# Kernel tuning notes

Hardware: AMD Instinct MI355X
Metric: run time of the kernel (lower is better)

## Reference

```python
import jax, jax.numpy as jnp
import numpy as np

B, D_IN, H = 4096, 2048, 2048


def setup_inputs() -> dict:
    key = jax.random.key(0)
    ks = jax.random.split(key, 8)
    s = 0.07
    return {
        "inputs": jax.random.normal(ks[0], (B, D_IN), dtype=jnp.float32),
        "state": jax.random.normal(ks[1], (B, H), dtype=jnp.float32),
        "theta_u_w": jax.random.uniform(ks[2], (H, H), jnp.float32, -s, s),
        "theta_w_w": jax.random.uniform(ks[3], (D_IN, H), jnp.float32, -s, s),
        "theta_w_b": jnp.ones((H,), jnp.float32),
        "eta_u_w": jax.random.uniform(ks[4], (H, H), jnp.float32, -s, s),
        "eta_w_w": jax.random.uniform(ks[5], (D_IN, H), jnp.float32, -s, s),
        "eta_w_b": -jnp.ones((H,), jnp.float32),
        "wx_w": jax.random.uniform(ks[6], (D_IN, H), jnp.float32, -s, s),
    }


def reference(inputs, state, theta_u_w, theta_w_w, theta_w_b,
              eta_u_w, eta_w_w, eta_w_b, wx_w):
    # Forget gate: sigmoid(state @ Wtu + inputs @ Wtw + btw)
    theta = jax.nn.sigmoid(state @ theta_u_w + inputs @ theta_w_w + theta_w_b)
    # Input gate: sigmoid(state @ Weu + inputs @ Wew + bew)
    eta = jax.nn.sigmoid(state @ eta_u_w + inputs @ eta_w_w + eta_w_b)
    Wx = inputs @ wx_w
    h = theta * jnp.tanh(state) + eta * jnp.tanh(Wx)
    return (h, h)
```

## Files before the change

kernel.cpp:

```cpp
#include <hip/hip_runtime.h>
#include <hip/hip_bf16.h>

#define BATCH 4096
#define KD    2048
#define HD    2048

typedef float f32x4 __attribute__((ext_vector_type(4)));
typedef short bf16x8 __attribute__((ext_vector_type(8)));

__device__ __forceinline__ unsigned short f2bf(float f) {
  unsigned int u = __builtin_bit_cast(unsigned int, f);
  u = (u + 0x7fffu + ((u >> 16) & 1u)) >> 16;
  return (unsigned short)u;
}

__device__ __forceinline__ float fsigmoid(float x) { return 1.0f / (1.0f + __expf(-x)); }
__device__ __forceinline__ float ftanh(float x) {
  return 1.0f - 2.0f / (__expf(2.0f * x) + 1.0f);
}

__device__ __forceinline__ void gload16(const void* g, void* l) {
  __builtin_amdgcn_global_load_lds(
      (const __attribute__((address_space(1))) unsigned int*)(uintptr_t)g,
      (__attribute__((address_space(3))) unsigned int*)(uintptr_t)l, 16, 0, 0);
}

#define WS_NEED   75497472ull
#define OFF_STATE (16ull << 20)
#define OFF_W     (32ull << 20)

__global__ __launch_bounds__(256) void act_convert(
    const float* __restrict__ inputs, const float* __restrict__ state,
    char* __restrict__ dst) {
  unsigned gid = blockIdx.x * 256 + threadIdx.x;
  const float* src = inputs;
  char* d = dst;
  unsigned id = gid;
  if (gid >= (1u << 20)) { src = state; d = dst + OFF_STATE; id = gid - (1u << 20); }
  const unsigned cid = id & 1023, panel = id >> 10;
  const unsigned kb = panel & 31, rb = panel >> 5;
  const unsigned x = cid * 16, r = x >> 7, xb = x & 127;
  const unsigned k0 = (xb ^ ((r & 7) << 4)) >> 1;
  const float* s = src + (size_t)(rb * 128 + r) * KD + kb * 64 + k0;
  const float4 v0 = *reinterpret_cast<const float4*>(s);
  const float4 v1 = *reinterpret_cast<const float4*>(s + 4);
  uint4 w;
  w.x = (unsigned)f2bf(v0.x) | ((unsigned)f2bf(v0.y) << 16);
  w.y = (unsigned)f2bf(v0.z) | ((unsigned)f2bf(v0.w) << 16);
  w.z = (unsigned)f2bf(v1.x) | ((unsigned)f2bf(v1.y) << 16);
  w.w = (unsigned)f2bf(v1.z) | ((unsigned)f2bf(v1.w) << 16);
  *reinterpret_cast<uint4*>(d + (size_t)id * 16) = w;
}

__global__ __launch_bounds__(256) void weight_convert(
    const float* __restrict__ tu, const float* __restrict__ eu,
    const float* __restrict__ tw, const float* __restrict__ ew,
    const float* __restrict__ xw, char* __restrict__ dst) {
  __shared__ float tile[64][129];
  const int tid = threadIdx.x;
  const int b = blockIdx.x;
  const int w = b >> 9, panel = b & 511;
  const int nb = panel >> 5, kb = panel & 31;
  const float* W = (w == 0) ? tu : (w == 1) ? eu : (w == 2) ? tw : (w == 3) ? ew : xw;
#pragma unroll
  for (int i = 0; i < 8; ++i) {
    const int idx = i * 256 + tid;
    const int row = idx >> 5, c4 = idx & 31;
    const float4 v = *reinterpret_cast<const float4*>(
        W + (size_t)(kb * 64 + row) * HD + nb * 128 + c4 * 4);
    tile[row][c4 * 4 + 0] = v.x; tile[row][c4 * 4 + 1] = v.y;
    tile[row][c4 * 4 + 2] = v.z; tile[row][c4 * 4 + 3] = v.w;
  }
  __syncthreads();
  char* d = dst + OFF_W + ((size_t)(w * 512 + panel) << 14);
#pragma unroll
  for (int i = 0; i < 4; ++i) {
    const int cid = i * 256 + tid;
    const int n = cid >> 3, xb = (cid & 7) * 16;
    const int k0 = (xb ^ ((n & 7) << 4)) >> 1;
    uint4 ww;
    ww.x = (unsigned)f2bf(tile[k0 + 0][n]) | ((unsigned)f2bf(tile[k0 + 1][n]) << 16);
    ww.y = (unsigned)f2bf(tile[k0 + 2][n]) | ((unsigned)f2bf(tile[k0 + 3][n]) << 16);
    ww.z = (unsigned)f2bf(tile[k0 + 4][n]) | ((unsigned)f2bf(tile[k0 + 5][n]) << 16);
    ww.w = (unsigned)f2bf(tile[k0 + 6][n]) | ((unsigned)f2bf(tile[k0 + 7][n]) << 16);
    *reinterpret_cast<uint4*>(d + n * 128 + xb) = ww;
  }
}

__global__ __launch_bounds__(256, 2) void cfn_main(
    const char* __restrict__ ws, const float* __restrict__ state,
    const float* __restrict__ th_b, const float* __restrict__ et_b,
    float* __restrict__ out) {
  __shared__ char sm[65536];
  const int tid = threadIdx.x;
  int bid = blockIdx.x;
  bid = (bid & 7) * 64 + (bid >> 3);
  const int bx = bid & 15, by = bid >> 4;
  const int lane = tid & 63, wv = tid >> 6;
  const int wr = wv >> 1, wc = wv & 1;
  const int lr = lane & 15, lg = lane >> 4;
  const int t16 = tid * 16;

  const char* pAx = ws;
  const char* pAs = ws + OFF_STATE;
  const char* pW  = ws + OFF_W;

  f32x4 at[4][4], ae[4][4], ax[4][4];
#pragma unroll
  for (int m = 0; m < 4; ++m)
#pragma unroll
    for (int n = 0; n < 4; ++n)
#pragma unroll
      for (int v = 0; v < 4; ++v) { at[m][n][v] = 0.f; ae[m][n][v] = 0.f; ax[m][n][v] = 0.f; }

  for (int kb = 0; kb < 32; ++kb) {
    const char* ga = pAs + ((size_t)(by * 32 + kb) << 14);
    const char* g0 = pW + ((size_t)(0 * 512 + bx * 32 + kb) << 14);
    const char* g1 = pW + ((size_t)(1 * 512 + bx * 32 + kb) << 14);
#pragma unroll
    for (int i = 0; i < 4; ++i) {
      gload16(ga + t16 + i * 4096, sm + t16 + i * 4096);
      gload16(g0 + t16 + i * 4096, sm + 16384 + t16 + i * 4096);
      gload16(g1 + t16 + i * 4096, sm + 32768 + t16 + i * 4096);
    }
    __syncthreads();
#pragma unroll
    for (int kk = 0; kk < 2; ++kk) {
      const int kc = kk * 64 + lg * 16;
      bf16x8 a[4], b[4];
#pragma unroll
      for (int m = 0; m < 4; ++m) {
        const int r = wr * 64 + m * 16 + lr;
        a[m] = *reinterpret_cast<const bf16x8*>(sm + r * 128 + (kc ^ ((r & 7) << 4)));
      }
#pragma unroll
      for (int n = 0; n < 4; ++n) {
        const int c = wc * 64 + n * 16 + lr;
        b[n] = *reinterpret_cast<const bf16x8*>(sm + 16384 + c * 128 + (kc ^ ((c & 7) << 4)));
      }
#pragma unroll
      for (int m = 0; m < 4; ++m)
#pragma unroll
        for (int n = 0; n < 4; ++n)
          at[m][n] = __builtin_amdgcn_mfma_f32_16x16x32_bf16(a[m], b[n], at[m][n], 0, 0, 0);
#pragma unroll
      for (int n = 0; n < 4; ++n) {
        const int c = wc * 64 + n * 16 + lr;
        b[n] = *reinterpret_cast<const bf16x8*>(sm + 32768 + c * 128 + (kc ^ ((c & 7) << 4)));
      }
#pragma unroll
      for (int m = 0; m < 4; ++m)
#pragma unroll
        for (int n = 0; n < 4; ++n)
          ae[m][n] = __builtin_amdgcn_mfma_f32_16x16x32_bf16(a[m], b[n], ae[m][n], 0, 0, 0);
    }
    __syncthreads();
  }

  for (int kb = 0; kb < 32; ++kb) {
    const char* ga = pAx + ((size_t)(by * 32 + kb) << 14);
    const char* g0 = pW + ((size_t)(2 * 512 + bx * 32 + kb) << 14);
    const char* g1 = pW + ((size_t)(3 * 512 + bx * 32 + kb) << 14);
    const char* g2 = pW + ((size_t)(4 * 512 + bx * 32 + kb) << 14);
#pragma unroll
    for (int i = 0; i < 4; ++i) {
      gload16(ga + t16 + i * 4096, sm + t16 + i * 4096);
      gload16(g0 + t16 + i * 4096, sm + 16384 + t16 + i * 4096);
      gload16(g1 + t16 + i * 4096, sm + 32768 + t16 + i * 4096);
      gload16(g2 + t16 + i * 4096, sm + 49152 + t16 + i * 4096);
    }
    __syncthreads();
#pragma unroll
    for (int kk = 0; kk < 2; ++kk) {
      const int kc = kk * 64 + lg * 16;
      bf16x8 a[4], b[4];
#pragma unroll
      for (int m = 0; m < 4; ++m) {
        const int r = wr * 64 + m * 16 + lr;
        a[m] = *reinterpret_cast<const bf16x8*>(sm + r * 128 + (kc ^ ((r & 7) << 4)));
      }
#pragma unroll
      for (int n = 0; n < 4; ++n) {
        const int c = wc * 64 + n * 16 + lr;
        b[n] = *reinterpret_cast<const bf16x8*>(sm + 16384 + c * 128 + (kc ^ ((c & 7) << 4)));
      }
#pragma unroll
      for (int m = 0; m < 4; ++m)
#pragma unroll
        for (int n = 0; n < 4; ++n)
          at[m][n] = __builtin_amdgcn_mfma_f32_16x16x32_bf16(a[m], b[n], at[m][n], 0, 0, 0);
#pragma unroll
      for (int n = 0; n < 4; ++n) {
        const int c = wc * 64 + n * 16 + lr;
        b[n] = *reinterpret_cast<const bf16x8*>(sm + 32768 + c * 128 + (kc ^ ((c & 7) << 4)));
      }
#pragma unroll
      for (int m = 0; m < 4; ++m)
#pragma unroll
        for (int n = 0; n < 4; ++n)
          ae[m][n] = __builtin_amdgcn_mfma_f32_16x16x32_bf16(a[m], b[n], ae[m][n], 0, 0, 0);
#pragma unroll
      for (int n = 0; n < 4; ++n) {
        const int c = wc * 64 + n * 16 + lr;
        b[n] = *reinterpret_cast<const bf16x8*>(sm + 49152 + c * 128 + (kc ^ ((c & 7) << 4)));
      }
#pragma unroll
      for (int m = 0; m < 4; ++m)
#pragma unroll
        for (int n = 0; n < 4; ++n)
          ax[m][n] = __builtin_amdgcn_mfma_f32_16x16x32_bf16(a[m], b[n], ax[m][n], 0, 0, 0);
    }
    __syncthreads();
  }

  float* const out2 = out + (size_t)BATCH * HD;
  const int n0 = bx * 128, m0 = by * 128;
#pragma unroll
  for (int n = 0; n < 4; ++n) {
    const int c = n0 + wc * 64 + n * 16 + lr;
    const float tb = th_b[c], eb = et_b[c];
#pragma unroll
    for (int m = 0; m < 4; ++m) {
#pragma unroll
      for (int v = 0; v < 4; ++v) {
        const int r = m0 + wr * 64 + m * 16 + lg * 4 + v;
        const float st = state[(size_t)r * HD + c];
        const float h = fsigmoid(at[m][n][v] + tb) * ftanh(st)
                      + fsigmoid(ae[m][n][v] + eb) * ftanh(ax[m][n][v]);
        out[(size_t)r * HD + c] = h;
        out2[(size_t)r * HD + c] = h;
      }
    }
  }
}

__global__ __launch_bounds__(256, 2) void cfn_fallback(
    const float* __restrict__ inputs, const float* __restrict__ state,
    const float* __restrict__ th_u, const float* __restrict__ th_w,
    const float* __restrict__ th_b, const float* __restrict__ et_u,
    const float* __restrict__ et_w, const float* __restrict__ et_b,
    const float* __restrict__ wx_w, float* __restrict__ out) {
  __shared__ unsigned short sA[128 * 64];
  __shared__ unsigned short sB[128 * 64];
  char* const sAb = (char*)sA;
  char* const sBb = (char*)sB;
  const int tid = threadIdx.x;
  const int n0 = blockIdx.x * 128;
  const int m0 = blockIdx.y * 128;
  const int lane = tid & 63, wv = tid >> 6;
  const int wr = wv >> 1, wc = wv & 1;
  const int lr = lane & 15, lg = lane >> 4;
  const int a_kq = tid & 15, a_mb = tid >> 4;
  const int b_n = tid & 127, b_k8 = (tid >> 7) * 8;
  f32x4 acc[4][4], r2[4][4];
  auto zero_acc = [&]() {
#pragma unroll
    for (int m = 0; m < 4; ++m)
#pragma unroll
      for (int n = 0; n < 4; ++n) {
        acc[m][n][0] = 0.f; acc[m][n][1] = 0.f; acc[m][n][2] = 0.f; acc[m][n][3] = 0.f;
      }
  };
  auto gemm_seg = [&](const float* __restrict__ Ap, const float* __restrict__ Wp) {
    for (int k0 = 0; k0 < KD; k0 += 64) {
#pragma unroll
      for (int p = 0; p < 8; ++p) {
        const int m = p * 16 + a_mb;
        const float4 v = *reinterpret_cast<const float4*>(
            Ap + (size_t)(m0 + m) * KD + k0 + a_kq * 4);
        uint2 w;
        w.x = (unsigned)f2bf(v.x) | ((unsigned)f2bf(v.y) << 16);
        w.y = (unsigned)f2bf(v.z) | ((unsigned)f2bf(v.w) << 16);
        const int byte = m * 128 + ((a_kq * 8) ^ ((m & 7) << 4));
        *reinterpret_cast<uint2*>(sAb + byte) = w;
      }
#pragma unroll
      for (int p = 0; p < 4; ++p) {
        const int kb = p * 16 + b_k8;
        const float* bp = Wp + (size_t)(k0 + kb) * HD + n0 + b_n;
        uint4 w;
        w.x = (unsigned)f2bf(bp[0 * HD]) | ((unsigned)f2bf(bp[1 * HD]) << 16);
        w.y = (unsigned)f2bf(bp[2 * HD]) | ((unsigned)f2bf(bp[3 * HD]) << 16);
        w.z = (unsigned)f2bf(bp[4 * HD]) | ((unsigned)f2bf(bp[5 * HD]) << 16);
        w.w = (unsigned)f2bf(bp[6 * HD]) | ((unsigned)f2bf(bp[7 * HD]) << 16);
        const int byte = b_n * 128 + ((kb * 2) ^ ((b_n & 7) << 4));
        *reinterpret_cast<uint4*>(sBb + byte) = w;
      }
      __syncthreads();
#pragma unroll
      for (int kk = 0; kk < 2; ++kk) {
        bf16x8 af[4], bfr[4];
#pragma unroll
        for (int m = 0; m < 4; ++m) {
          const int r = wr * 64 + m * 16 + lr;
          af[m] = *reinterpret_cast<const bf16x8*>(sAb + r * 128 + ((kk * 64 + lg * 16) ^ ((r & 7) << 4)));
        }
#pragma unroll
        for (int n = 0; n < 4; ++n) {
          const int c = wc * 64 + n * 16 + lr;
          bfr[n] = *reinterpret_cast<const bf16x8*>(sBb + c * 128 + ((kk * 64 + lg * 16) ^ ((c & 7) << 4)));
        }
#pragma unroll
        for (int m = 0; m < 4; ++m)
#pragma unroll
          for (int n = 0; n < 4; ++n)
            acc[m][n] = __builtin_amdgcn_mfma_f32_16x16x32_bf16(af[m], bfr[n], acc[m][n], 0, 0, 0);
      }
      __syncthreads();
    }
  };
  zero_acc();
  gemm_seg(state, et_u);
  gemm_seg(inputs, et_w);
#pragma unroll
  for (int n = 0; n < 4; ++n) {
    const int c = n0 + wc * 64 + n * 16 + lr;
    const float eb = et_b[c];
#pragma unroll
    for (int m = 0; m < 4; ++m)
#pragma unroll
      for (int v = 0; v < 4; ++v) r2[m][n][v] = fsigmoid(acc[m][n][v] + eb);
  }
  zero_acc();
  gemm_seg(inputs, wx_w);
#pragma unroll
  for (int m = 0; m < 4; ++m)
#pragma unroll
    for (int n = 0; n < 4; ++n)
#pragma unroll
      for (int v = 0; v < 4; ++v) r2[m][n][v] *= ftanh(acc[m][n][v]);
  zero_acc();
  gemm_seg(state, th_u);
  gemm_seg(inputs, th_w);
  float* const out2 = out + (size_t)BATCH * HD;
#pragma unroll
  for (int n = 0; n < 4; ++n) {
    const int c = n0 + wc * 64 + n * 16 + lr;
    const float tb = th_b[c];
#pragma unroll
    for (int m = 0; m < 4; ++m)
#pragma unroll
      for (int v = 0; v < 4; ++v) {
        const int r = m0 + wr * 64 + m * 16 + lg * 4 + v;
        const float st = state[(size_t)r * HD + c];
        const float h = fsigmoid(acc[m][n][v] + tb) * ftanh(st) + r2[m][n][v];
        out[(size_t)r * HD + c] = h;
        out2[(size_t)r * HD + c] = h;
      }
  }
}

extern "C" void kernel_launch(void* const* d_in, const int* in_sizes, int n_in,
                              void* d_out, int out_size, void* d_ws, size_t ws_size,
                              hipStream_t stream) {
  const float* inputs = (const float*)d_in[0];
  const float* state  = (const float*)d_in[1];
  const float* th_u   = (const float*)d_in[2];
  const float* th_w   = (const float*)d_in[3];
  const float* th_b   = (const float*)d_in[4];
  const float* et_u   = (const float*)d_in[5];
  const float* et_w   = (const float*)d_in[6];
  const float* et_b   = (const float*)d_in[7];
  const float* wx_w   = (const float*)d_in[8];
  float* out = (float*)d_out;

  if (ws_size < WS_NEED) {
    dim3 grid(HD / 128, BATCH / 128);
    hipLaunchKernelGGL(cfn_fallback, grid, dim3(256), 0, stream,
                       inputs, state, th_u, th_w, th_b, et_u, et_w, et_b, wx_w, out);
    return;
  }

  char* ws = (char*)d_ws;
  hipLaunchKernelGGL(act_convert, dim3(8192), dim3(256), 0, stream, inputs, state, ws);
  hipLaunchKernelGGL(weight_convert, dim3(2560), dim3(256), 0, stream,
                     th_u, et_u, th_w, et_w, wx_w, ws);
  hipLaunchKernelGGL(cfn_main, dim3(512), dim3(256), 0, stream,
                     ws, state, th_b, et_b, out);
}
```

Measured before the change: 189.8 us.

## Enlarge main GEMM tile to 256x128 with 512 threads and double-buffered LDS

```diff
diff --git a/kernel.cpp b/kernel.cpp
--- a/kernel.cpp
+++ b/kernel.cpp
@@ -87,17 +87,17 @@
   }
 }
 
-__global__ __launch_bounds__(256, 2) void cfn_main(
+__global__ __launch_bounds__(512, 2) void cfn_main(
     const char* __restrict__ ws, const float* __restrict__ state,
     const float* __restrict__ th_b, const float* __restrict__ et_b,
     float* __restrict__ out) {
-  __shared__ char sm[65536];
+  __shared__ char sm[163840];
   const int tid = threadIdx.x;
   int bid = blockIdx.x;
-  bid = (bid & 7) * 64 + (bid >> 3);
+  bid = (bid & 7) * 32 + (bid >> 3);
   const int bx = bid & 15, by = bid >> 4;
   const int lane = tid & 63, wv = tid >> 6;
-  const int wr = wv >> 1, wc = wv & 1;
+  const int wm = wv >> 2, wn = wv & 3;
   const int lr = lane & 15, lg = lane >> 4;
   const int t16 = tid * 16;
 
@@ -105,125 +105,119 @@
   const char* pAs = ws + OFF_STATE;
   const char* pW  = ws + OFF_W;
 
-  f32x4 at[4][4], ae[4][4], ax[4][4];
-#pragma unroll
-  for (int m = 0; m < 4; ++m)
-#pragma unroll
-    for (int n = 0; n < 4; ++n)
+  f32x4 at[8][2], ae[8][2], ax[8][2];
+#pragma unroll
+  for (int m = 0; m < 8; ++m)
+#pragma unroll
+    for (int n = 0; n < 2; ++n)
 #pragma unroll
       for (int v = 0; v < 4; ++v) { at[m][n][v] = 0.f; ae[m][n][v] = 0.f; ax[m][n][v] = 0.f; }
 
-  for (int kb = 0; kb < 32; ++kb) {
-    const char* ga = pAs + ((size_t)(by * 32 + kb) << 14);
-    const char* g0 = pW + ((size_t)(0 * 512 + bx * 32 + kb) << 14);
-    const char* g1 = pW + ((size_t)(1 * 512 + bx * 32 + kb) << 14);
-#pragma unroll
-    for (int i = 0; i < 4; ++i) {
-      gload16(ga + t16 + i * 4096, sm + t16 + i * 4096);
-      gload16(g0 + t16 + i * 4096, sm + 16384 + t16 + i * 4096);
-      gload16(g1 + t16 + i * 4096, sm + 32768 + t16 + i * 4096);
-    }
+  auto stage = [&](int t, char* dst) {
+    const int kb = t & 31;
+    const char* Asrc = (t < 32) ? pAs : pAx;
+    const int w0 = (t < 32) ? 0 : 2;
+    const int nB = (t < 32) ? 2 : 3;
+    const char* pa = Asrc + (((size_t)(by * 64 + kb)) << 14);
+#pragma unroll
+    for (int s = 0; s < 2; ++s)
+#pragma unroll
+      for (int j = 0; j < 2; ++j)
+        gload16(pa + s * (32 << 14) + t16 + j * 8192,
+                dst + s * 16384 + t16 + j * 8192);
+#pragma unroll
+    for (int p = 0; p < 3; ++p) {
+      if (p < nB) {
+        const char* pb = pW + (((size_t)((w0 + p) * 512 + bx * 32 + kb)) << 14);
+#pragma unroll
+        for (int j = 0; j < 2; ++j)
+          gload16(pb + t16 + j * 8192, dst + 32768 + p * 16384 + t16 + j * 8192);
+      }
+    }
+  };
+
+  auto compute2 = [&](const char* buf) {
+#pragma unroll
+    for (int kk = 0; kk < 2; ++kk) {
+      const int swz = (kk * 64 + lg * 16) ^ ((lr & 7) << 4);
+      bf16x8 b0[2], b1[2];
+#pragma unroll
+      for (int n = 0; n < 2; ++n) {
+        const int c = wn * 32 + n * 16 + lr;
+        b0[n] = *reinterpret_cast<const bf16x8*>(buf + 32768 + c * 128 + swz);
+        b1[n] = *reinterpret_cast<const bf16x8*>(buf + 49152 + c * 128 + swz);
+      }
+#pragma unroll
+      for (int m = 0; m < 8; ++m) {
+        const int r = wm * 128 + m * 16 + lr;
+        const bf16x8 a = *reinterpret_cast<const bf16x8*>(buf + r * 128 + swz);
+#pragma unroll
+        for (int n = 0; n < 2; ++n) {
+          at[m][n] = __builtin_amdgcn_mfma_f32_16x16x32_bf16(a, b0[n], at[m][n], 0, 0, 0);
+          ae[m][n] = __builtin_amdgcn_mfma_f32_16x16x32_bf16(a, b1[n], ae[m][n], 0, 0, 0);
+        }
+      }
+    }
+  };
+
+  auto compute3 = [&](const char* buf) {
+#pragma unroll
+    for (int kk = 0; kk < 2; ++kk) {
+      const int swz = (kk * 64 + lg * 16) ^ ((lr & 7) << 4);
+      bf16x8 b0[2], b1[2], b2[2];
+#pragma unroll
+      for (int n = 0; n < 2; ++n) {
+        const int c = wn * 32 + n * 16 + lr;
+        b0[n] = *reinterpret_cast<const bf16x8*>(buf + 32768 + c * 128 + swz);
+        b1[n] = *reinterpret_cast<const bf16x8*>(buf + 49152 + c * 128 + swz);
+        b2[n] = *reinterpret_cast<const bf16x8*>(buf + 65536 + c * 128 + swz);
+      }
+#pragma unroll
+      for (int m = 0; m < 8; ++m) {
+        const int r = wm * 128 + m * 16 + lr;
+        const bf16x8 a = *reinterpret_cast<const bf16x8*>(buf + r * 128 + swz);
+#pragma unroll
+        for (int n = 0; n < 2; ++n) {
+          at[m][n] = __builtin_amdgcn_mfma_f32_16x16x32_bf16(a, b0[n], at[m][n], 0, 0, 0);
+          ae[m][n] = __builtin_amdgcn_mfma_f32_16x16x32_bf16(a, b1[n], ae[m][n], 0, 0, 0);
+          ax[m][n] = __builtin_amdgcn_mfma_f32_16x16x32_bf16(a, b2[n], ax[m][n], 0, 0, 0);
+        }
+      }
+    }
+  };
+
+  char* cur = sm;
+  char* nxt = sm + 81920;
+  stage(0, cur);
+  __syncthreads();
+
+  for (int t = 0; t < 32; ++t) {
+    stage(t + 1, nxt);
+    compute2(cur);
+    asm volatile("s_waitcnt vmcnt(0)" ::: "memory");
     __syncthreads();
-#pragma unroll
-    for (int kk = 0; kk < 2; ++kk) {
-      const int kc = kk * 64 + lg * 16;
-      bf16x8 a[4], b[4];
-#pragma unroll
-      for (int m = 0; m < 4; ++m) {
-        const int r = wr * 64 + m * 16 + lr;
-        a[m] = *reinterpret_cast<const bf16x8*>(sm + r * 128 + (kc ^ ((r & 7) << 4)));
-      }
-#pragma unroll
-      for (int n = 0; n < 4; ++n) {
-        const int c = wc * 64 + n * 16 + lr;
-        b[n] = *reinterpret_cast<const bf16x8*>(sm + 16384 + c * 128 + (kc ^ ((c & 7) << 4)));
-      }
-#pragma unroll
-      for (int m = 0; m < 4; ++m)
-#pragma unroll
-        for (int n = 0; n < 4; ++n)
-          at[m][n] = __builtin_amdgcn_mfma_f32_16x16x32_bf16(a[m], b[n], at[m][n], 0, 0, 0);
-#pragma unroll
-      for (int n = 0; n < 4; ++n) {
-        const int c = wc * 64 + n * 16 + lr;
-        b[n] = *reinterpret_cast<const bf16x8*>(sm + 32768 + c * 128 + (kc ^ ((c & 7) << 4)));
-      }
-#pragma unroll
-      for (int m = 0; m < 4; ++m)
-#pragma unroll
-        for (int n = 0; n < 4; ++n)
-          ae[m][n] = __builtin_amdgcn_mfma_f32_16x16x32_bf16(a[m], b[n], ae[m][n], 0, 0, 0);
-    }
+    char* tmp = cur; cur = nxt; nxt = tmp;
+  }
+  for (int t = 32; t < 64; ++t) {
+    if (t < 63) stage(t + 1, nxt);
+    compute3(cur);
+    asm volatile("s_waitcnt vmcnt(0)" ::: "memory");
     __syncthreads();
-  }
-
-  for (int kb = 0; kb < 32; ++kb) {
-    const char* ga = pAx + ((size_t)(by * 32 + kb) << 14);
-    const char* g0 = pW + ((size_t)(2 * 512 + bx * 32 + kb) << 14);
-    const char* g1 = pW + ((size_t)(3 * 512 + bx * 32 + kb) << 14);
-    const char* g2 = pW + ((size_t)(4 * 512 + bx * 32 + kb) << 14);
-#pragma unroll
-    for (int i = 0; i < 4; ++i) {
-      gload16(ga + t16 + i * 4096, sm + t16 + i * 4096);
-      gload16(g0 + t16 + i * 4096, sm + 16384 + t16 + i * 4096);
-      gload16(g1 + t16 + i * 4096, sm + 32768 + t16 + i * 4096);
-      gload16(g2 + t16 + i * 4096, sm + 49152 + t16 + i * 4096);
-    }
-    __syncthreads();
-#pragma unroll
-    for (int kk = 0; kk < 2; ++kk) {
-      const int kc = kk * 64 + lg * 16;
-      bf16x8 a[4], b[4];
-#pragma unroll
-      for (int m = 0; m < 4; ++m) {
-        const int r = wr * 64 + m * 16 + lr;
-        a[m] = *reinterpret_cast<const bf16x8*>(sm + r * 128 + (kc ^ ((r & 7) << 4)));
-      }
-#pragma unroll
-      for (int n = 0; n < 4; ++n) {
-        const int c = wc * 64 + n * 16 + lr;
-        b[n] = *reinterpret_cast<const bf16x8*>(sm + 16384 + c * 128 + (kc ^ ((c & 7) << 4)));
-      }
-#pragma unroll
-      for (int m = 0; m < 4; ++m)
-#pragma unroll
-        for (int n = 0; n < 4; ++n)
-          at[m][n] = __builtin_amdgcn_mfma_f32_16x16x32_bf16(a[m], b[n], at[m][n], 0, 0, 0);
-#pragma unroll
-      for (int n = 0; n < 4; ++n) {
-        const int c = wc * 64 + n * 16 + lr;
-        b[n] = *reinterpret_cast<const bf16x8*>(sm + 32768 + c * 128 + (kc ^ ((c & 7) << 4)));
-      }
-#pragma unroll
-      for (int m = 0; m < 4; ++m)
-#pragma unroll
-        for (int n = 0; n < 4; ++n)
-          ae[m][n] = __builtin_amdgcn_mfma_f32_16x16x32_bf16(a[m], b[n], ae[m][n], 0, 0, 0);
-#pragma unroll
-      for (int n = 0; n < 4; ++n) {
-        const int c = wc * 64 + n * 16 + lr;
-        b[n] = *reinterpret_cast<const bf16x8*>(sm + 49152 + c * 128 + (kc ^ ((c & 7) << 4)));
-      }
-#pragma unroll
-      for (int m = 0; m < 4; ++m)
-#pragma unroll
-        for (int n = 0; n < 4; ++n)
-          ax[m][n] = __builtin_amdgcn_mfma_f32_16x16x32_bf16(a[m], b[n], ax[m][n], 0, 0, 0);
-    }
-    __syncthreads();
+    char* tmp = cur; cur = nxt; nxt = tmp;
   }
 
   float* const out2 = out + (size_t)BATCH * HD;
-  const int n0 = bx * 128, m0 = by * 128;
-#pragma unroll
-  for (int n = 0; n < 4; ++n) {
-    const int c = n0 + wc * 64 + n * 16 + lr;
+  const int n0 = bx * 128 + wn * 32;
+  const int m0 = by * 256 + wm * 128;
+#pragma unroll
+  for (int n = 0; n < 2; ++n) {
+    const int c = n0 + n * 16 + lr;
     const float tb = th_b[c], eb = et_b[c];
 #pragma unroll
-    for (int m = 0; m < 4; ++m) {
+    for (int m = 0; m < 8; ++m) {
 #pragma unroll
       for (int v = 0; v < 4; ++v) {
-        const int r = m0 + wr * 64 + m * 16 + lg * 4 + v;
+        const int r = m0 + m * 16 + lg * 4 + v;
         const float st = state[(size_t)r * HD + c];
         const float h = fsigmoid(at[m][n][v] + tb) * ftanh(st)
                       + fsigmoid(ae[m][n][v] + eb) * ftanh(ax[m][n][v]);
@@ -375,6 +369,6 @@
   hipLaunchKernelGGL(act_convert, dim3(8192), dim3(256), 0, stream, inputs, state, ws);
   hipLaunchKernelGGL(weight_convert, dim3(2560), dim3(256), 0, stream,
                      th_u, et_u, th_w, et_w, wx_w, ws);
-  hipLaunchKernelGGL(cfn_main, dim3(512), dim3(256), 0, stream,
+  hipLaunchKernelGGL(cfn_main, dim3(256), dim3(512), 0, stream,
                      ws, state, th_b, et_b, out);
 }
```

Measured after the change: 202.3 us. 1.07x slower.

## Double-buffer LDS with 32-wide K panels to overlap loads and MFMA

Applied to the files above, without the earlier changes.

```diff
diff --git a/kernel.cpp b/kernel.cpp
--- a/kernel.cpp
+++ b/kernel.cpp
@@ -37,11 +37,11 @@
   char* d = dst;
   unsigned id = gid;
   if (gid >= (1u << 20)) { src = state; d = dst + OFF_STATE; id = gid - (1u << 20); }
-  const unsigned cid = id & 1023, panel = id >> 10;
-  const unsigned kb = panel & 31, rb = panel >> 5;
-  const unsigned x = cid * 16, r = x >> 7, xb = x & 127;
-  const unsigned k0 = (xb ^ ((r & 7) << 4)) >> 1;
-  const float* s = src + (size_t)(rb * 128 + r) * KD + kb * 64 + k0;
+  const unsigned cid = id & 511, panel = id >> 9;
+  const unsigned kb = panel & 63, rb = panel >> 6;
+  const unsigned x = cid * 16, r = x >> 6, xb = x & 63;
+  const unsigned k0 = (xb ^ ((r & 3) << 4)) >> 1;
+  const float* s = src + (size_t)(rb * 128 + r) * KD + kb * 32 + k0;
   const float4 v0 = *reinterpret_cast<const float4*>(s);
   const float4 v1 = *reinterpret_cast<const float4*>(s + 4);
   uint4 w;
@@ -59,31 +59,33 @@
   __shared__ float tile[64][129];
   const int tid = threadIdx.x;
   const int b = blockIdx.x;
-  const int w = b >> 9, panel = b & 511;
-  const int nb = panel >> 5, kb = panel & 31;
+  const int w = b >> 9, blk = b & 511;
+  const int nb = blk >> 5, kb2 = blk & 31;
   const float* W = (w == 0) ? tu : (w == 1) ? eu : (w == 2) ? tw : (w == 3) ? ew : xw;
 #pragma unroll
   for (int i = 0; i < 8; ++i) {
     const int idx = i * 256 + tid;
     const int row = idx >> 5, c4 = idx & 31;
     const float4 v = *reinterpret_cast<const float4*>(
-        W + (size_t)(kb * 64 + row) * HD + nb * 128 + c4 * 4);
+        W + (size_t)(kb2 * 64 + row) * HD + nb * 128 + c4 * 4);
     tile[row][c4 * 4 + 0] = v.x; tile[row][c4 * 4 + 1] = v.y;
     tile[row][c4 * 4 + 2] = v.z; tile[row][c4 * 4 + 3] = v.w;
   }
   __syncthreads();
-  char* d = dst + OFF_W + ((size_t)(w * 512 + panel) << 14);
 #pragma unroll
   for (int i = 0; i < 4; ++i) {
-    const int cid = i * 256 + tid;
-    const int n = cid >> 3, xb = (cid & 7) * 16;
-    const int k0 = (xb ^ ((n & 7) << 4)) >> 1;
+    const int cg = i * 256 + tid;
+    const int half = cg >> 9, cid = cg & 511;
+    const int n = cid >> 2, xb = (cid & 3) * 16;
+    const int k0 = (xb ^ ((n & 3) << 4)) >> 1;
+    char* d = dst + OFF_W +
+        ((size_t)(w * 1024 + nb * 64 + kb2 * 2 + half) << 13);
     uint4 ww;
-    ww.x = (unsigned)f2bf(tile[k0 + 0][n]) | ((unsigned)f2bf(tile[k0 + 1][n]) << 16);
-    ww.y = (unsigned)f2bf(tile[k0 + 2][n]) | ((unsigned)f2bf(tile[k0 + 3][n]) << 16);
-    ww.z = (unsigned)f2bf(tile[k0 + 4][n]) | ((unsigned)f2bf(tile[k0 + 5][n]) << 16);
-    ww.w = (unsigned)f2bf(tile[k0 + 6][n]) | ((unsigned)f2bf(tile[k0 + 7][n]) << 16);
-    *reinterpret_cast<uint4*>(d + n * 128 + xb) = ww;
+    ww.x = (unsigned)f2bf(tile[half * 32 + k0 + 0][n]) | ((unsigned)f2bf(tile[half * 32 + k0 + 1][n]) << 16);
+    ww.y = (unsigned)f2bf(tile[half * 32 + k0 + 2][n]) | ((unsigned)f2bf(tile[half * 32 + k0 + 3][n]) << 16);
+    ww.z = (unsigned)f2bf(tile[half * 32 + k0 + 4][n]) | ((unsigned)f2bf(tile[half * 32 + k0 + 5][n]) << 16);
+    ww.w = (unsigned)f2bf(tile[half * 32 + k0 + 6][n]) | ((unsigned)f2bf(tile[half * 32 + k0 + 7][n]) << 16);
+    *reinterpret_cast<uint4*>(d + n * 64 + xb) = ww;
   }
 }
 
@@ -100,6 +102,7 @@
   const int wr = wv >> 1, wc = wv & 1;
   const int lr = lane & 15, lg = lane >> 4;
   const int t16 = tid * 16;
+  const int swz = (lg * 16) ^ ((lr & 3) << 4);
 
   const char* pAx = ws;
   const char* pAs = ws + OFF_STATE;
@@ -113,105 +116,88 @@
 #pragma unroll
       for (int v = 0; v < 4; ++v) { at[m][n][v] = 0.f; ae[m][n][v] = 0.f; ax[m][n][v] = 0.f; }
 
-  for (int kb = 0; kb < 32; ++kb) {
-    const char* ga = pAs + ((size_t)(by * 32 + kb) << 14);
-    const char* g0 = pW + ((size_t)(0 * 512 + bx * 32 + kb) << 14);
-    const char* g1 = pW + ((size_t)(1 * 512 + bx * 32 + kb) << 14);
-#pragma unroll
-    for (int i = 0; i < 4; ++i) {
-      gload16(ga + t16 + i * 4096, sm + t16 + i * 4096);
-      gload16(g0 + t16 + i * 4096, sm + 16384 + t16 + i * 4096);
-      gload16(g1 + t16 + i * 4096, sm + 32768 + t16 + i * 4096);
-    }
+  auto stage = [&](int t, char* dst) {
+    const int kb = t & 63;
+    const char* Asrc = (t < 64) ? pAs : pAx;
+    const int w0 = (t < 64) ? 0 : 2;
+    const int nB = (t < 64) ? 2 : 3;
+    const char* pa = Asrc + ((size_t)(by * 64 + kb) << 13);
+    gload16(pa + t16, dst + t16);
+    gload16(pa + t16 + 4096, dst + t16 + 4096);
+#pragma unroll
+    for (int p = 0; p < 3; ++p) {
+      if (p < nB) {
+        const char* pb = pW + ((size_t)((w0 + p) * 1024 + bx * 64 + kb) << 13);
+        gload16(pb + t16, dst + 8192 + p * 8192 + t16);
+        gload16(pb + t16 + 4096, dst + 8192 + p * 8192 + t16 + 4096);
+      }
+    }
+  };
+
+  auto compute2 = [&](const char* buf) {
+    bf16x8 a[4], b0[4], b1[4];
+#pragma unroll
+    for (int m = 0; m < 4; ++m) {
+      const int r = wr * 64 + m * 16 + lr;
+      a[m] = *reinterpret_cast<const bf16x8*>(buf + r * 64 + swz);
+    }
+#pragma unroll
+    for (int n = 0; n < 4; ++n) {
+      const int c = wc * 64 + n * 16 + lr;
+      b0[n] = *reinterpret_cast<const bf16x8*>(buf + 8192 + c * 64 + swz);
+      b1[n] = *reinterpret_cast<const bf16x8*>(buf + 16384 + c * 64 + swz);
+    }
+#pragma unroll
+    for (int m = 0; m < 4; ++m)
+#pragma unroll
+      for (int n = 0; n < 4; ++n) {
+        at[m][n] = __builtin_amdgcn_mfma_f32_16x16x32_bf16(a[m], b0[n], at[m][n], 0, 0, 0);
+        ae[m][n] = __builtin_amdgcn_mfma_f32_16x16x32_bf16(a[m], b1[n], ae[m][n], 0, 0, 0);
+      }
+  };
+
+  auto compute3 = [&](const char* buf) {
+    bf16x8 a[4], b0[4], b1[4], b2[4];
+#pragma unroll
+    for (int m = 0; m < 4; ++m) {
+      const int r = wr * 64 + m * 16 + lr;
+      a[m] = *reinterpret_cast<const bf16x8*>(buf + r * 64 + swz);
+    }
+#pragma unroll
+    for (int n = 0; n < 4; ++n) {
+      const int c = wc * 64 + n * 16 + lr;
+      b0[n] = *reinterpret_cast<const bf16x8*>(buf + 8192 + c * 64 + swz);
+      b1[n] = *reinterpret_cast<const bf16x8*>(buf + 16384 + c * 64 + swz);
+      b2[n] = *reinterpret_cast<const bf16x8*>(buf + 24576 + c * 64 + swz);
+    }
+#pragma unroll
+    for (int m = 0; m < 4; ++m)
+#pragma unroll
+      for (int n = 0; n < 4; ++n) {
+        at[m][n] = __builtin_amdgcn_mfma_f32_16x16x32_bf16(a[m], b0[n], at[m][n], 0, 0, 0);
+        ae[m][n] = __builtin_amdgcn_mfma_f32_16x16x32_bf16(a[m], b1[n], ae[m][n], 0, 0, 0);
+        ax[m][n] = __builtin_amdgcn_mfma_f32_16x16x32_bf16(a[m], b2[n], ax[m][n], 0, 0, 0);
+      }
+  };
+
+  char* cur = sm;
+  char* nxt = sm + 32768;
+  stage(0, cur);
+  __syncthreads();
+
+  for (int t = 0; t < 64; ++t) {
+    stage(t + 1, nxt);
+    compute2(cur);
     __syncthreads();
-#pragma unroll
-    for (int kk = 0; kk < 2; ++kk) {
-      const int kc = kk * 64 + lg * 16;
-      bf16x8 a[4], b[4];
-#pragma unroll
-      for (int m = 0; m < 4; ++m) {
-        const int r = wr * 64 + m * 16 + lr;
-        a[m] = *reinterpret_cast<const bf16x8*>(sm + r * 128 + (kc ^ ((r & 7) << 4)));
-      }
-#pragma unroll
-      for (int n = 0; n < 4; ++n) {
-        const int c = wc * 64 + n * 16 + lr;
-        b[n] = *reinterpret_cast<const bf16x8*>(sm + 16384 + c * 128 + (kc ^ ((c & 7) << 4)));
-      }
-#pragma unroll
-      for (int m = 0; m < 4; ++m)
-#pragma unroll
-        for (int n = 0; n < 4; ++n)
-          at[m][n] = __builtin_amdgcn_mfma_f32_16x16x32_bf16(a[m], b[n], at[m][n], 0, 0, 0);
-#pragma unroll
-      for (int n = 0; n < 4; ++n) {
-        const int c = wc * 64 + n * 16 + lr;
-        b[n] = *reinterpret_cast<const bf16x8*>(sm + 32768 + c * 128 + (kc ^ ((c & 7) << 4)));
-      }
-#pragma unroll
-      for (int m = 0; m < 4; ++m)
-#pragma unroll
-        for (int n = 0; n < 4; ++n)
-          ae[m][n] = __builtin_amdgcn_mfma_f32_16x16x32_bf16(a[m], b[n], ae[m][n], 0, 0, 0);
-    }
+    char* tmp = cur; cur = nxt; nxt = tmp;
+  }
+  for (int t = 64; t < 127; ++t) {
+    stage(t + 1, nxt);
+    compute3(cur);
     __syncthreads();
-  }
-
-  for (int kb = 0; kb < 32; ++kb) {
-    const char* ga = pAx + ((size_t)(by * 32 + kb) << 14);
-    const char* g0 = pW + ((size_t)(2 * 512 + bx * 32 + kb) << 14);
-    const char* g1 = pW + ((size_t)(3 * 512 + bx * 32 + kb) << 14);
-    const char* g2 = pW + ((size_t)(4 * 512 + bx * 32 + kb) << 14);
-#pragma unroll
-    for (int i = 0; i < 4; ++i) {
-      gload16(ga + t16 + i * 4096, sm + t16 + i * 4096);
-      gload16(g0 + t16 + i * 4096, sm + 16384 + t16 + i * 4096);
-      gload16(g1 + t16 + i * 4096, sm + 32768 + t16 + i * 4096);
-      gload16(g2 + t16 + i * 4096, sm + 49152 + t16 + i * 4096);
-    }
-    __syncthreads();
-#pragma unroll
-    for (int kk = 0; kk < 2; ++kk) {
-      const int kc = kk * 64 + lg * 16;
-      bf16x8 a[4], b[4];
-#pragma unroll
-      for (int m = 0; m < 4; ++m) {
-        const int r = wr * 64 + m * 16 + lr;
-        a[m] = *reinterpret_cast<const bf16x8*>(sm + r * 128 + (kc ^ ((r & 7) << 4)));
-      }
-#pragma unroll
-      for (int n = 0; n < 4; ++n) {
-        const int c = wc * 64 + n * 16 + lr;
-        b[n] = *reinterpret_cast<const bf16x8*>(sm + 16384 + c * 128 + (kc ^ ((c & 7) << 4)));
-      }
-#pragma unroll
-      for (int m = 0; m < 4; ++m)
-#pragma unroll
-        for (int n = 0; n < 4; ++n)
-          at[m][n] = __builtin_amdgcn_mfma_f32_16x16x32_bf16(a[m], b[n], at[m][n], 0, 0, 0);
-#pragma unroll
-      for (int n = 0; n < 4; ++n) {
-        const int c = wc * 64 + n * 16 + lr;
-        b[n] = *reinterpret_cast<const bf16x8*>(sm + 32768 + c * 128 + (kc ^ ((c & 7) << 4)));
-      }
-#pragma unroll
-      for (int m = 0; m < 4; ++m)
-#pragma unroll
-        for (int n = 0; n < 4; ++n)
-          ae[m][n] = __builtin_amdgcn_mfma_f32_16x16x32_bf16(a[m], b[n], ae[m][n], 0, 0, 0);
-#pragma unroll
-      for (int n = 0; n < 4; ++n) {
-        const int c = wc * 64 + n * 16 + lr;
-        b[n] = *reinterpret_cast<const bf16x8*>(sm + 49152 + c * 128 + (kc ^ ((c & 7) << 4)));
-      }
-#pragma unroll
-      for (int m = 0; m < 4; ++m)
-#pragma unroll
-        for (int n = 0; n < 4; ++n)
-          ax[m][n] = __builtin_amdgcn_mfma_f32_16x16x32_bf16(a[m], b[n], ax[m][n], 0, 0, 0);
-    }
-    __syncthreads();
-  }
+    char* tmp = cur; cur = nxt; nxt = tmp;
+  }
+  compute3(cur);
 
   float* const out2 = out + (size_t)BATCH * HD;
   const int n0 = bx * 128, m0 = by * 128;
```

Result: slower. 229.6 us (+21.0%).
